# Kernel tuning notes

Measured on AMD Instinct MI355X. Metric: run time of the kernel, lower is better.

The kernel has to match this reference:

```python
import jax, jax.numpy as jnp
import numpy as np
from jax import lax

B, D, N, M = 512, 1024, 8192, 2048  # batch, input_dim, n_sdr, n_minicolumns
K = 4            # n_columns
W_SPARSE = 320   # SDR sparsity w (active bits per SDR)
K_ACTIVE = 40    # active minicolumns per step
PERM_THRESH = 0.5
LR = 0.01
CONSENSUS_THRESH = 1.0  # strict AND


def setup_inputs() -> dict:
    key = jax.random.key(0)
    k1, k2, k3 = jax.random.split(key, 3)
    s_batch = jax.random.normal(k1, (B, D), dtype=jnp.float32)
    W_enc = jax.random.normal(k2, (K, D, N), dtype=jnp.float32)  # per-column encoders (no weight sharing)
    perm = jax.random.uniform(k3, (K, M, N), dtype=jnp.float32)  # per-column permanences
    return {"s_batch": s_batch, "W_enc": W_enc, "perm": perm}


def _one_hot_topk(scores, k):
    # scores: [B, C] -> binary [B, C] with top-k per row set to 1
    _, idx = lax.top_k(scores, k)
    rows = jnp.arange(scores.shape[0])[:, None]
    return jnp.zeros_like(scores).at[rows, idx].set(1.0)


def reference(s_batch, W_enc, perm):
    def column(We, P):
        # SDRSpace.encode: random projection + top-w binarization
        scores = s_batch @ We                       # [B, N]
        sdr = _one_hot_topk(scores, W_SPARSE)       # [B, N] binary
        # SpatialPooler.forward_batch: overlap with connected synapses, top-k minicolumns
        connected = (P >= PERM_THRESH).astype(sdr.dtype)  # [M, N]
        overlap = sdr @ connected.T                 # [B, M]
        act = _one_hot_topk(overlap, K_ACTIVE)      # [B, M] binary winners
        # hebbian_update_batch: reinforce active inputs, punish inactive, on winning columns
        delta = (LR / B) * (act.T @ (2.0 * sdr - 1.0))    # [M, N] scatter-accumulated
        P_new = jnp.clip(P + delta, 0.0, 1.0)
        return sdr, P_new

    all_sdrs, perms_new = jax.vmap(column)(W_enc, perm)   # [K,B,N], [K,M,N]
    vote_fraction = all_sdrs.mean(axis=0)                  # [B, N]
    consensus = (vote_fraction >= CONSENSUS_THRESH).astype(jnp.float32)
    return consensus, all_sdrs[0], perms_new
```

## Files before the change

### kernel.cpp

```cpp
#include <hip/hip_runtime.h>
#include <stdint.h>

#define B_   512
#define D_   1024
#define N_   8192
#define M_   2048
#define K_   4
#define WSP  320
#define KACT 40
#define NW   128

typedef _Float16 f16;
typedef _Float16 f16x4 __attribute__((ext_vector_type(4)));
typedef _Float16 f16x8 __attribute__((ext_vector_type(8)));
typedef float f32x4 __attribute__((ext_vector_type(4)));

#define BM 128
#define BN 128
#define SPLIT_SCALE 2048.0f
#define SPLIT_INV (1.0f / 2048.0f)

#define GLD16(g, l) __builtin_amdgcn_global_load_lds( \
    (const __attribute__((address_space(1))) uint32_t*)(g), \
    (__attribute__((address_space(3))) uint32_t*)(l), 16, 0, 0)

__global__ __launch_bounds__(256) void conn_bits_kernel(const float* __restrict__ perm,
                                                        uint32_t* __restrict__ conn32,
                                                        int* __restrict__ mcount) {
    int km = blockIdx.x;
    int tid = threadIdx.x;
    if (tid == 0) mcount[km] = 0;
    const float* p = perm + (size_t)km * N_ + tid * 32;
    uint32_t bits = 0;
#pragma unroll
    for (int q = 0; q < 8; q++) {
        float4 v = *(const float4*)&p[q * 4];
        bits |= (v.x >= 0.5f ? 1u : 0u) << (q * 4 + 0);
        bits |= (v.y >= 0.5f ? 1u : 0u) << (q * 4 + 1);
        bits |= (v.z >= 0.5f ? 1u : 0u) << (q * 4 + 2);
        bits |= (v.w >= 0.5f ? 1u : 0u) << (q * 4 + 3);
    }
    conn32[(size_t)km * 256 + tid] = bits;
}

__global__ __launch_bounds__(256) void splitS_kernel(const float* __restrict__ S,
                                                     uint8_t* __restrict__ imgA) {
    int blk = blockIdx.x;
    int mt = blk >> 5, dstep = blk & 31;
    int tid = threadIdx.x;
    uint8_t* outb = imgA + (size_t)blk * 16384;
#pragma unroll
    for (int q = 0; q < 4; q++) {
        int o = tid * 16 + q * 4096;
        int r = o >> 7, inner = o & 127;
        int sw = (r & 7) << 4;
        int raw = inner ^ sw;
        int plane = raw >> 6;
        int k0 = (raw & 63) >> 1;
        const float* sp = &S[(size_t)(mt * 128 + r) * D_ + dstep * 32 + k0];
        float4 v0 = *(const float4*)sp;
        float4 v1 = *(const float4*)(sp + 4);
        f16x8 out;
        if (plane == 0) {
            out[0] = (f16)v0.x; out[1] = (f16)v0.y; out[2] = (f16)v0.z; out[3] = (f16)v0.w;
            out[4] = (f16)v1.x; out[5] = (f16)v1.y; out[6] = (f16)v1.z; out[7] = (f16)v1.w;
        } else {
            f16 h0 = (f16)v0.x, h1 = (f16)v0.y, h2 = (f16)v0.z, h3 = (f16)v0.w;
            f16 h4 = (f16)v1.x, h5 = (f16)v1.y, h6 = (f16)v1.z, h7 = (f16)v1.w;
            out[0] = (f16)((v0.x - (float)h0) * SPLIT_SCALE);
            out[1] = (f16)((v0.y - (float)h1) * SPLIT_SCALE);
            out[2] = (f16)((v0.z - (float)h2) * SPLIT_SCALE);
            out[3] = (f16)((v0.w - (float)h3) * SPLIT_SCALE);
            out[4] = (f16)((v1.x - (float)h4) * SPLIT_SCALE);
            out[5] = (f16)((v1.y - (float)h5) * SPLIT_SCALE);
            out[6] = (f16)((v1.z - (float)h6) * SPLIT_SCALE);
            out[7] = (f16)((v1.w - (float)h7) * SPLIT_SCALE);
        }
        *(f16x8*)&outb[o] = out;
    }
}

__device__ __forceinline__ uint32_t packHL(float x) {
    f16 h = (f16)x;
    f16 l = (f16)((x - (float)h) * SPLIT_SCALE);
    union { f16 v[2]; uint32_t u; } c;
    c.v[0] = h; c.v[1] = l;
    return c.u;
}

__global__ __launch_bounds__(256, 2) void gemm_kernel(const uint8_t* __restrict__ imgA,
                                                      const float* __restrict__ W,
                                                      float* __restrict__ C) {
    __shared__ __align__(16) uint8_t Alds[16384];
    __shared__ __align__(16) uint8_t Blds[16384];

    int bid = blockIdx.x;
    int l = (bid & 7) * 128 + (bid >> 3);
    int mt = l & 3, nt = (l >> 2) & 63, kt = l >> 8;

    int tid = threadIdx.x;
    int wave = tid >> 6, lane = tid & 63;
    int wm = wave >> 1, wn = wave & 1;
    int lr = lane & 15, lg = lane >> 4;

    const uint8_t* srcA = imgA + (size_t)(mt * 32) * 16384 + wave * 1024 + lane * 16;
    uint8_t* dstA = Alds + wave * 1024;

    const float* Wp = W + (size_t)kt * D_ * N_ + nt * BN;
    float* Cp = C + (size_t)kt * B_ * N_ + (size_t)(mt * BM) * N_ + nt * BN;

    int bn = tid & 127;
    int kc0 = tid >> 7;
    int bsw = (bn & 7) << 4;

    f32x4 acc0[4][4], acc1[4][4];
#pragma unroll
    for (int i = 0; i < 4; i++)
#pragma unroll
        for (int j = 0; j < 4; j++) {
            acc0[i][j] = (f32x4){0.f, 0.f, 0.f, 0.f};
            acc1[i][j] = (f32x4){0.f, 0.f, 0.f, 0.f};
        }

    for (int dstep = 0; dstep < 32; dstep++) {
#pragma unroll
        for (int q = 0; q < 4; q++)
            GLD16(srcA + q * 4096, dstA + q * 4096);
        srcA += 16384;
#pragma unroll
        for (int kci = 0; kci < 2; kci++) {
            int kc = kc0 + kci * 2;
            const float* wp = Wp + (size_t)(dstep * 32 + kc * 8) * N_ + bn;
            float w0 = wp[0 * N_], w1 = wp[1 * N_], w2 = wp[2 * N_], w3 = wp[3 * N_];
            float w4 = wp[4 * N_], w5 = wp[5 * N_], w6 = wp[6 * N_], w7 = wp[7 * N_];
            f16x8 hv, lv;
            hv[0] = (f16)w0; hv[1] = (f16)w1; hv[2] = (f16)w2; hv[3] = (f16)w3;
            hv[4] = (f16)w4; hv[5] = (f16)w5; hv[6] = (f16)w6; hv[7] = (f16)w7;
            lv[0] = (f16)((w0 - (float)hv[0]) * SPLIT_SCALE);
            lv[1] = (f16)((w1 - (float)hv[1]) * SPLIT_SCALE);
            lv[2] = (f16)((w2 - (float)hv[2]) * SPLIT_SCALE);
            lv[3] = (f16)((w3 - (float)hv[3]) * SPLIT_SCALE);
            lv[4] = (f16)((w4 - (float)hv[4]) * SPLIT_SCALE);
            lv[5] = (f16)((w5 - (float)hv[5]) * SPLIT_SCALE);
            lv[6] = (f16)((w6 - (float)hv[6]) * SPLIT_SCALE);
            lv[7] = (f16)((w7 - (float)hv[7]) * SPLIT_SCALE);
            *(f16x8*)&Blds[bn * 128 + ((kc * 16) ^ bsw)] = hv;
            *(f16x8*)&Blds[bn * 128 + ((64 + kc * 16) ^ bsw)] = lv;
        }
        __syncthreads();

        f16x8 ah[4], al[4];
#pragma unroll
        for (int i = 0; i < 4; i++) {
            int r = wm * 64 + i * 16 + lr;
            int sw = (r & 7) << 4;
            ah[i] = *(const f16x8*)&Alds[r * 128 + ((lg * 16) ^ sw)];
            al[i] = *(const f16x8*)&Alds[r * 128 + ((64 + lg * 16) ^ sw)];
        }
#pragma unroll
        for (int jj = 0; jj < 4; jj++) {
            int n = wn * 64 + jj * 16 + lr;
            int sw = (n & 7) << 4;
            f16x8 bh = *(const f16x8*)&Blds[n * 128 + ((lg * 16) ^ sw)];
            f16x8 bl = *(const f16x8*)&Blds[n * 128 + ((64 + lg * 16) ^ sw)];
#pragma unroll
            for (int i = 0; i < 4; i++) {
                acc0[i][jj] = __builtin_amdgcn_mfma_f32_16x16x32_f16(ah[i], bh, acc0[i][jj], 0, 0, 0);
                acc1[i][jj] = __builtin_amdgcn_mfma_f32_16x16x32_f16(ah[i], bl, acc1[i][jj], 0, 0, 0);
                acc1[i][jj] = __builtin_amdgcn_mfma_f32_16x16x32_f16(al[i], bh, acc1[i][jj], 0, 0, 0);
            }
        }
        __syncthreads();
    }
#pragma unroll
    for (int i = 0; i < 4; i++)
#pragma unroll
        for (int jj = 0; jj < 4; jj++) {
            int r0 = wm * 64 + i * 16 + lg * 4;
            int c0 = wn * 64 + jj * 16 + lr;
#pragma unroll
            for (int r = 0; r < 4; r++)
                Cp[(size_t)(r0 + r) * N_ + c0] = acc0[i][jj][r] + acc1[i][jj][r] * SPLIT_INV;
        }
}

__global__ __launch_bounds__(256) void sdr_select_kernel(const float* __restrict__ scores,
                                                         uint32_t* __restrict__ sdr_bits32) {
    __shared__ int hist[256];
    __shared__ int scan2[256];
    __shared__ uint32_t sh_prefix;
    __shared__ int sh_r;

    int b = blockIdx.x;
    int k = blockIdx.y;
    int tid = threadIdx.x;
    const float* row = scores + ((size_t)k * B_ + b) * N_ + tid * 32;

    uint32_t key[32];
#pragma unroll
    for (int q = 0; q < 8; q++) {
        float4 v = *(const float4*)&row[q * 4];
        uint32_t u0 = __float_as_uint(v.x), u1 = __float_as_uint(v.y);
        uint32_t u2 = __float_as_uint(v.z), u3 = __float_as_uint(v.w);
        key[q * 4 + 0] = (u0 & 0x80000000u) ? ~u0 : (u0 | 0x80000000u);
        key[q * 4 + 1] = (u1 & 0x80000000u) ? ~u1 : (u1 | 0x80000000u);
        key[q * 4 + 2] = (u2 & 0x80000000u) ? ~u2 : (u2 | 0x80000000u);
        key[q * 4 + 3] = (u3 & 0x80000000u) ? ~u3 : (u3 | 0x80000000u);
    }
    if (tid == 0) { sh_prefix = 0u; sh_r = WSP; }
    __syncthreads();

    for (int p = 3; p >= 0; p--) {
        hist[tid] = 0;
        __syncthreads();
        uint32_t prefix = sh_prefix;
        int r = sh_r;
        uint32_t maskHi = (p == 3) ? 0u : (0xFFFFFFFFu << ((p + 1) * 8));
        int shift = p * 8;
#pragma unroll
        for (int j = 0; j < 32; j++) {
            uint32_t u = key[j];
            if ((u & maskHi) == prefix) atomicAdd(&hist[(u >> shift) & 255], 1);
        }
        __syncthreads();
#pragma unroll
        for (int off = 1; off < 256; off <<= 1) {
            int x = hist[tid] + ((tid + off < 256) ? hist[tid + off] : 0);
            __syncthreads();
            hist[tid] = x;
            __syncthreads();
        }
        int Sv = hist[tid];
        int Sn = (tid < 255) ? hist[tid + 1] : 0;
        if (Sv >= r && Sn < r) { sh_prefix = prefix | ((uint32_t)tid << shift); sh_r = r - Sn; }
        __syncthreads();
    }
    uint32_t t = sh_prefix;

    int gt = 0, eq = 0;
#pragma unroll
    for (int j = 0; j < 32; j++) {
        gt += (key[j] > t); eq += (key[j] == t);
    }
    hist[tid] = gt; scan2[tid] = eq;
    __syncthreads();
#pragma unroll
    for (int off = 1; off < 256; off <<= 1) {
        int g = hist[tid] + ((tid >= off) ? hist[tid - off] : 0);
        int e = scan2[tid] + ((tid >= off) ? scan2[tid - off] : 0);
        __syncthreads();
        hist[tid] = g; scan2[tid] = e;
        __syncthreads();
    }
    int totalGt = hist[255];
    int eb = scan2[tid] - eq;
    int r_eq = WSP - totalGt;

    uint32_t bits = 0;
#pragma unroll
    for (int j = 0; j < 32; j++) {
        uint32_t u = key[j];
        bool f = (u > t) || ((u == t) && (eb < r_eq));
        if (u == t) eb++;
        if (f) bits |= (1u << j);
    }
    sdr_bits32[((size_t)k * B_ + b) * 256 + tid] = bits;
}

#define OV_BBLK 16
#define OV_MTILE 512
__global__ __launch_bounds__(256) void overlap_mat_kernel(const uint64_t* __restrict__ sdr_bits,
                                                          const uint64_t* __restrict__ conn,
                                                          uint16_t* __restrict__ ovmat) {
    __shared__ uint64_t sw[OV_BBLK][NW];

    int bid = blockIdx.x;
    int nb = (bid & 7) * 64 + (bid >> 3);
    int k = nb >> 7;
    int rem = nb & 127;
    int b0 = (rem >> 2) * OV_BBLK;
    int m0 = (rem & 3) * OV_MTILE;
    int tid = threadIdx.x;

    for (int i = tid; i < OV_BBLK * NW; i += 256) {
        int bb = i >> 7, w = i & 127;
        sw[bb][w] = sdr_bits[((size_t)k * B_ + b0 + bb) * NW + w];
    }
    __syncthreads();

    int m_a = m0 + tid;
    int m_b = m0 + tid + 256;
    const ulonglong2* cra = (const ulonglong2*)(conn + ((size_t)k * M_ + m_a) * NW);
    const ulonglong2* crb = (const ulonglong2*)(conn + ((size_t)k * M_ + m_b) * NW);

    int acca[OV_BBLK], accb[OV_BBLK];
#pragma unroll
    for (int i = 0; i < OV_BBLK; i++) { acca[i] = 0; accb[i] = 0; }

#pragma unroll 2
    for (int wp = 0; wp < NW / 2; wp++) {
        ulonglong2 ca = cra[wp];
        ulonglong2 cb = crb[wp];
#pragma unroll
        for (int bb = 0; bb < OV_BBLK; bb++) {
            ulonglong2 s = *(const ulonglong2*)&sw[bb][wp * 2];
            acca[bb] += __popcll(ca.x & s.x) + __popcll(ca.y & s.y);
            accb[bb] += __popcll(cb.x & s.x) + __popcll(cb.y & s.y);
        }
    }
#pragma unroll
    for (int bb = 0; bb < OV_BBLK; bb++) {
        ovmat[((size_t)k * B_ + b0 + bb) * M_ + m_a] = (uint16_t)acca[bb];
        ovmat[((size_t)k * B_ + b0 + bb) * M_ + m_b] = (uint16_t)accb[bb];
    }
}

__global__ __launch_bounds__(256) void top40_kernel(const uint16_t* __restrict__ ovmat,
                                                    int* __restrict__ mcount,
                                                    int* __restrict__ mlist) {
    __shared__ int hist[512];
    __shared__ int scanbuf[256];
    __shared__ int sh_t, sh_req;

    int kb = blockIdx.x;
    int k = kb >> 9;
    int b = kb & 511;
    int tid = threadIdx.x;

    union { uint4 raw; uint16_t v[8]; } ov;
    ov.raw = *(const uint4*)&ovmat[(size_t)kb * M_ + tid * 8];

    hist[tid] = 0; hist[tid + 256] = 0;
    __syncthreads();
#pragma unroll
    for (int j = 0; j < 8; j++) atomicAdd(&hist[ov.v[j]], 1);
    __syncthreads();
#pragma unroll
    for (int off = 1; off < 512; off <<= 1) {
        int a0 = hist[tid] + ((tid + off < 512) ? hist[tid + off] : 0);
        int a1 = hist[tid + 256] + ((tid + 256 + off < 512) ? hist[tid + 256 + off] : 0);
        __syncthreads();
        hist[tid] = a0; hist[tid + 256] = a1;
        __syncthreads();
    }
#pragma unroll
    for (int which = 0; which < 2; which++) {
        int v = tid + which * 256;
        int Sv = hist[v];
        int Sn = (v < 511) ? hist[v + 1] : 0;
        if (Sv >= KACT && Sn < KACT) { sh_t = v; sh_req = KACT - Sn; }
    }
    __syncthreads();
    int t = sh_t, req = sh_req;
    int eq = 0;
#pragma unroll
    for (int j = 0; j < 8; j++) eq += (ov.v[j] == t);
    scanbuf[tid] = eq;
    __syncthreads();
#pragma unroll
    for (int off = 1; off < 256; off <<= 1) {
        int e = scanbuf[tid] + ((tid >= off) ? scanbuf[tid - off] : 0);
        __syncthreads();
        scanbuf[tid] = e;
        __syncthreads();
    }
    int eb = scanbuf[tid] - eq;
#pragma unroll
    for (int j = 0; j < 8; j++) {
        int m = tid * 8 + j;
        int v2 = ov.v[j];
        bool act = (v2 > t) || (v2 == t && eb < req);
        if (v2 == t) eb++;
        if (act) {
            int pos = atomicAdd(&mcount[k * M_ + m], 1);
            mlist[(((size_t)k * M_ + m) << 9) + pos] = b;
        }
    }
}

__global__ void consensus_kernel(const uint64_t* __restrict__ sdr_bits,
                                 float* __restrict__ cons,
                                 float* __restrict__ sdr0) {
    int gid = blockIdx.x * 256 + threadIdx.x;
    int b = gid >> 13;
    int n = gid & (N_ - 1);
    int wi = n >> 6, bit = n & 63;
    size_t base = (size_t)b * NW + wi;
    uint64_t w0 = sdr_bits[base];
    uint64_t w1 = sdr_bits[(size_t)1 * B_ * NW + base];
    uint64_t w2 = sdr_bits[(size_t)2 * B_ * NW + base];
    uint64_t w3 = sdr_bits[(size_t)3 * B_ * NW + base];
    uint64_t a = w0 & w1 & w2 & w3;
    cons[gid] = (float)((a >> bit) & 1);
    sdr0[gid] = (float)((w0 >> bit) & 1);
}

__global__ __launch_bounds__(512) void update_kernel(const float* __restrict__ perm,
                                                     const uint64_t* __restrict__ sdr_bits,
                                                     const int* __restrict__ mcount,
                                                     const int* __restrict__ mlist,
                                                     float* __restrict__ pout) {
    __shared__ int blist[512];
    int km = blockIdx.x;
    int k = km / M_;
    int tid = threadIdx.x;
    int cnt = mcount[km];
    for (int i = tid; i < cnt; i += 512) blist[i] = mlist[((size_t)km << 9) + i];
    __syncthreads();

    int n0 = tid * 16;
    int c[16];
#pragma unroll
    for (int j = 0; j < 16; j++) c[j] = 0;
    int wi = n0 >> 6;
    int sh = n0 & 63;
    const uint64_t* sb = sdr_bits + (size_t)k * B_ * NW;
    for (int i = 0; i < cnt; i++) {
        uint64_t wv = sb[(size_t)blist[i] * NW + wi];
        unsigned bits = (unsigned)((wv >> sh) & 0xFFFFu);
#pragma unroll
        for (int j = 0; j < 16; j++) c[j] += (bits >> j) & 1;
    }
    const float scale = (float)(0.01 / 512.0);
    const float* pr = perm + (size_t)km * N_ + n0;
    float* po = pout + (size_t)km * N_ + n0;
#pragma unroll
    for (int q = 0; q < 4; q++) {
        float4 pv = *(const float4*)&pr[q * 4];
        float4 o;
        o.x = fminf(fmaxf(pv.x + scale * (float)(2 * c[q * 4 + 0] - cnt), 0.f), 1.f);
        o.y = fminf(fmaxf(pv.y + scale * (float)(2 * c[q * 4 + 1] - cnt), 0.f), 1.f);
        o.z = fminf(fmaxf(pv.z + scale * (float)(2 * c[q * 4 + 2] - cnt), 0.f), 1.f);
        o.w = fminf(fmaxf(pv.w + scale * (float)(2 * c[q * 4 + 3] - cnt), 0.f), 1.f);
        *(float4*)&po[q * 4] = o;
    }
}

extern "C" void kernel_launch(void* const* d_in, const int* in_sizes, int n_in,
                              void* d_out, int out_size, void* d_ws, size_t ws_size,
                              hipStream_t stream) {
    const float* s_batch = (const float*)d_in[0];
    const float* W_enc   = (const float*)d_in[1];
    const float* perm    = (const float*)d_in[2];

    float* out  = (float*)d_out;
    float* cons = out;
    float* sdr0 = out + (size_t)B_ * N_;
    float* pout = out + (size_t)2 * B_ * N_;

    char* ws = (char*)d_ws;
    float*    scores   = (float*)ws;
    uint16_t* ovmat    = (uint16_t*)ws;
    uint64_t* sdr_bits = (uint64_t*)(ws + ((size_t)64 << 20));
    uint64_t* conn     = (uint64_t*)(ws + ((size_t)66 << 20));
    int*      mcount   = (int*)(ws + ((size_t)74 << 20));
    int*      mlist    = (int*)(ws + ((size_t)75 << 20));
    uint8_t*  imgA     = (uint8_t*)(ws + ((size_t)92 << 20));

    conn_bits_kernel<<<K_ * M_, 256, 0, stream>>>(perm, (uint32_t*)conn, mcount);

    splitS_kernel<<<4 * 32, 256, 0, stream>>>(s_batch, imgA);

    gemm_kernel<<<K_ * (B_ / BM) * (N_ / BN), 256, 0, stream>>>(imgA, W_enc, scores);

    dim3 gs(B_, K_);
    sdr_select_kernel<<<gs, 256, 0, stream>>>(scores, (uint32_t*)sdr_bits);

    overlap_mat_kernel<<<K_ * (B_ / OV_BBLK) * (M_ / OV_MTILE), 256, 0, stream>>>(
        sdr_bits, conn, ovmat);
    top40_kernel<<<K_ * B_, 256, 0, stream>>>(ovmat, mcount, mlist);

    consensus_kernel<<<(B_ * N_) / 256, 256, 0, stream>>>(sdr_bits, cons, sdr0);
    update_kernel<<<K_ * M_, 512, 0, stream>>>(perm, sdr_bits, mcount, mlist, pout);
}
```

Before: 474.0 us.

## Double-buffer the split-f16 GEMM with wider tiles and merge small launches

```diff
diff --git a/kernel.cpp b/kernel.cpp
--- a/kernel.cpp
+++ b/kernel.cpp
@@ -16,7 +16,7 @@
 typedef float f32x4 __attribute__((ext_vector_type(4)));
 
 #define BM 128
-#define BN 128
+#define BN 256
 #define SPLIT_SCALE 2048.0f
 #define SPLIT_INV (1.0f / 2048.0f)
 
@@ -24,11 +24,49 @@
     (const __attribute__((address_space(1))) uint32_t*)(g), \
     (__attribute__((address_space(3))) uint32_t*)(l), 16, 0, 0)
 
-__global__ __launch_bounds__(256) void conn_bits_kernel(const float* __restrict__ perm,
-                                                        uint32_t* __restrict__ conn32,
-                                                        int* __restrict__ mcount) {
-    int km = blockIdx.x;
-    int tid = threadIdx.x;
+__global__ __launch_bounds__(256) void prep_kernel(const float* __restrict__ perm,
+                                                   uint32_t* __restrict__ conn32,
+                                                   int* __restrict__ mcount,
+                                                   const float* __restrict__ S,
+                                                   uint8_t* __restrict__ imgA) {
+    int bid = blockIdx.x;
+    int tid = threadIdx.x;
+    if (bid < 128) {
+        int blk = bid;
+        int mt = blk >> 5, dstep = blk & 31;
+        uint8_t* outb = imgA + (size_t)blk * 16384;
+#pragma unroll
+        for (int q = 0; q < 4; q++) {
+            int o = tid * 16 + q * 4096;
+            int r = o >> 7, inner = o & 127;
+            int sw = (r & 7) << 4;
+            int raw = inner ^ sw;
+            int plane = raw >> 6;
+            int k0 = (raw & 63) >> 1;
+            const float* sp = &S[(size_t)(mt * 128 + r) * D_ + dstep * 32 + k0];
+            float4 v0 = *(const float4*)sp;
+            float4 v1 = *(const float4*)(sp + 4);
+            f16x8 out;
+            if (plane == 0) {
+                out[0] = (f16)v0.x; out[1] = (f16)v0.y; out[2] = (f16)v0.z; out[3] = (f16)v0.w;
+                out[4] = (f16)v1.x; out[5] = (f16)v1.y; out[6] = (f16)v1.z; out[7] = (f16)v1.w;
+            } else {
+                f16 h0 = (f16)v0.x, h1 = (f16)v0.y, h2 = (f16)v0.z, h3 = (f16)v0.w;
+                f16 h4 = (f16)v1.x, h5 = (f16)v1.y, h6 = (f16)v1.z, h7 = (f16)v1.w;
+                out[0] = (f16)((v0.x - (float)h0) * SPLIT_SCALE);
+                out[1] = (f16)((v0.y - (float)h1) * SPLIT_SCALE);
+                out[2] = (f16)((v0.z - (float)h2) * SPLIT_SCALE);
+                out[3] = (f16)((v0.w - (float)h3) * SPLIT_SCALE);
+                out[4] = (f16)((v1.x - (float)h4) * SPLIT_SCALE);
+                out[5] = (f16)((v1.y - (float)h5) * SPLIT_SCALE);
+                out[6] = (f16)((v1.z - (float)h6) * SPLIT_SCALE);
+                out[7] = (f16)((v1.w - (float)h7) * SPLIT_SCALE);
+            }
+            *(f16x8*)&outb[o] = out;
+        }
+        return;
+    }
+    int km = bid - 128;
     if (tid == 0) mcount[km] = 0;
     const float* p = perm + (size_t)km * N_ + tid * 32;
     uint32_t bits = 0;
@@ -43,74 +81,45 @@
     conn32[(size_t)km * 256 + tid] = bits;
 }
 
-__global__ __launch_bounds__(256) void splitS_kernel(const float* __restrict__ S,
-                                                     uint8_t* __restrict__ imgA) {
-    int blk = blockIdx.x;
-    int mt = blk >> 5, dstep = blk & 31;
-    int tid = threadIdx.x;
-    uint8_t* outb = imgA + (size_t)blk * 16384;
-#pragma unroll
-    for (int q = 0; q < 4; q++) {
-        int o = tid * 16 + q * 4096;
-        int r = o >> 7, inner = o & 127;
-        int sw = (r & 7) << 4;
-        int raw = inner ^ sw;
-        int plane = raw >> 6;
-        int k0 = (raw & 63) >> 1;
-        const float* sp = &S[(size_t)(mt * 128 + r) * D_ + dstep * 32 + k0];
-        float4 v0 = *(const float4*)sp;
-        float4 v1 = *(const float4*)(sp + 4);
-        f16x8 out;
-        if (plane == 0) {
-            out[0] = (f16)v0.x; out[1] = (f16)v0.y; out[2] = (f16)v0.z; out[3] = (f16)v0.w;
-            out[4] = (f16)v1.x; out[5] = (f16)v1.y; out[6] = (f16)v1.z; out[7] = (f16)v1.w;
-        } else {
-            f16 h0 = (f16)v0.x, h1 = (f16)v0.y, h2 = (f16)v0.z, h3 = (f16)v0.w;
-            f16 h4 = (f16)v1.x, h5 = (f16)v1.y, h6 = (f16)v1.z, h7 = (f16)v1.w;
-            out[0] = (f16)((v0.x - (float)h0) * SPLIT_SCALE);
-            out[1] = (f16)((v0.y - (float)h1) * SPLIT_SCALE);
-            out[2] = (f16)((v0.z - (float)h2) * SPLIT_SCALE);
-            out[3] = (f16)((v0.w - (float)h3) * SPLIT_SCALE);
-            out[4] = (f16)((v1.x - (float)h4) * SPLIT_SCALE);
-            out[5] = (f16)((v1.y - (float)h5) * SPLIT_SCALE);
-            out[6] = (f16)((v1.z - (float)h6) * SPLIT_SCALE);
-            out[7] = (f16)((v1.w - (float)h7) * SPLIT_SCALE);
-        }
-        *(f16x8*)&outb[o] = out;
-    }
-}
-
-__device__ __forceinline__ uint32_t packHL(float x) {
-    f16 h = (f16)x;
-    f16 l = (f16)((x - (float)h) * SPLIT_SCALE);
-    union { f16 v[2]; uint32_t u; } c;
-    c.v[0] = h; c.v[1] = l;
-    return c.u;
-}
-
-__global__ __launch_bounds__(256, 2) void gemm_kernel(const uint8_t* __restrict__ imgA,
+__device__ __forceinline__ void pack_write_B(uint8_t* Bn, const float* w,
+                                             int kc0, int bn, int bsw) {
+#pragma unroll
+    for (int kci = 0; kci < 2; kci++) {
+        int kc = kc0 * 2 + kci;
+        f16x8 hv, lv;
+#pragma unroll
+        for (int j = 0; j < 8; j++) {
+            float x = w[kci * 8 + j];
+            f16 h = (f16)x;
+            hv[j] = h;
+            lv[j] = (f16)((x - (float)h) * SPLIT_SCALE);
+        }
+        *(f16x8*)&Bn[bn * 128 + ((kc * 16) ^ bsw)] = hv;
+        *(f16x8*)&Bn[bn * 128 + ((64 + kc * 16) ^ bsw)] = lv;
+    }
+}
+
+__global__ __launch_bounds__(512, 2) void gemm_kernel(const uint8_t* __restrict__ imgA,
                                                       const float* __restrict__ W,
                                                       float* __restrict__ C) {
-    __shared__ __align__(16) uint8_t Alds[16384];
-    __shared__ __align__(16) uint8_t Blds[16384];
+    __shared__ __align__(16) uint8_t lds[98304];
 
     int bid = blockIdx.x;
-    int l = (bid & 7) * 128 + (bid >> 3);
-    int mt = l & 3, nt = (l >> 2) & 63, kt = l >> 8;
+    int l = (bid & 7) * 64 + (bid >> 3);
+    int mt = l & 3, nt = (l >> 2) & 31, kt = l >> 7;
 
     int tid = threadIdx.x;
     int wave = tid >> 6, lane = tid & 63;
-    int wm = wave >> 1, wn = wave & 1;
+    int wm = wave >> 2, wn = wave & 3;
     int lr = lane & 15, lg = lane >> 4;
 
-    const uint8_t* srcA = imgA + (size_t)(mt * 32) * 16384 + wave * 1024 + lane * 16;
-    uint8_t* dstA = Alds + wave * 1024;
+    const uint8_t* srcA0 = imgA + (size_t)(mt * 32) * 16384 + wave * 1024 + lane * 16;
 
     const float* Wp = W + (size_t)kt * D_ * N_ + nt * BN;
     float* Cp = C + (size_t)kt * B_ * N_ + (size_t)(mt * BM) * N_ + nt * BN;
 
-    int bn = tid & 127;
-    int kc0 = tid >> 7;
+    int bn = tid & 255;
+    int kc0 = tid >> 8;
     int bsw = (bn & 7) << 4;
 
     f32x4 acc0[4][4], acc1[4][4];
@@ -122,56 +131,65 @@
             acc1[i][j] = (f32x4){0.f, 0.f, 0.f, 0.f};
         }
 
+    {
+        uint8_t* dA = lds + wave * 1024;
+        GLD16(srcA0, dA);
+        GLD16(srcA0 + 8192, dA + 8192);
+        float w[16];
+        const float* wp0 = Wp + (size_t)(kc0 * 16) * N_ + bn;
+#pragma unroll
+        for (int j = 0; j < 16; j++) w[j] = wp0[(size_t)j * N_];
+        pack_write_B(lds + 32768, w, kc0, bn, bsw);
+    }
+    __syncthreads();
+
     for (int dstep = 0; dstep < 32; dstep++) {
-#pragma unroll
-        for (int q = 0; q < 4; q++)
-            GLD16(srcA + q * 4096, dstA + q * 4096);
-        srcA += 16384;
-#pragma unroll
-        for (int kci = 0; kci < 2; kci++) {
-            int kc = kc0 + kci * 2;
-            const float* wp = Wp + (size_t)(dstep * 32 + kc * 8) * N_ + bn;
-            float w0 = wp[0 * N_], w1 = wp[1 * N_], w2 = wp[2 * N_], w3 = wp[3 * N_];
-            float w4 = wp[4 * N_], w5 = wp[5 * N_], w6 = wp[6 * N_], w7 = wp[7 * N_];
-            f16x8 hv, lv;
-            hv[0] = (f16)w0; hv[1] = (f16)w1; hv[2] = (f16)w2; hv[3] = (f16)w3;
-            hv[4] = (f16)w4; hv[5] = (f16)w5; hv[6] = (f16)w6; hv[7] = (f16)w7;
-            lv[0] = (f16)((w0 - (float)hv[0]) * SPLIT_SCALE);
-            lv[1] = (f16)((w1 - (float)hv[1]) * SPLIT_SCALE);
-            lv[2] = (f16)((w2 - (float)hv[2]) * SPLIT_SCALE);
-            lv[3] = (f16)((w3 - (float)hv[3]) * SPLIT_SCALE);
-            lv[4] = (f16)((w4 - (float)hv[4]) * SPLIT_SCALE);
-            lv[5] = (f16)((w5 - (float)hv[5]) * SPLIT_SCALE);
-            lv[6] = (f16)((w6 - (float)hv[6]) * SPLIT_SCALE);
-            lv[7] = (f16)((w7 - (float)hv[7]) * SPLIT_SCALE);
-            *(f16x8*)&Blds[bn * 128 + ((kc * 16) ^ bsw)] = hv;
-            *(f16x8*)&Blds[bn * 128 + ((64 + kc * 16) ^ bsw)] = lv;
-        }
-        __syncthreads();
+        int cur = dstep & 1;
+        uint8_t* Ac = lds + cur * 16384;
+        uint8_t* Bc = lds + 32768 + cur * 32768;
+        bool pf = (dstep < 31);
+
+        float wreg[16];
+        if (pf) {
+            const uint8_t* sA = srcA0 + (size_t)(dstep + 1) * 16384;
+            uint8_t* dA = lds + (cur ^ 1) * 16384 + wave * 1024;
+            GLD16(sA, dA);
+            GLD16(sA + 8192, dA + 8192);
+            const float* wp0 = Wp + (size_t)((dstep + 1) * 32 + kc0 * 16) * N_ + bn;
+#pragma unroll
+            for (int j = 0; j < 16; j++) wreg[j] = wp0[(size_t)j * N_];
+        }
 
         f16x8 ah[4], al[4];
 #pragma unroll
         for (int i = 0; i < 4; i++) {
             int r = wm * 64 + i * 16 + lr;
             int sw = (r & 7) << 4;
-            ah[i] = *(const f16x8*)&Alds[r * 128 + ((lg * 16) ^ sw)];
-            al[i] = *(const f16x8*)&Alds[r * 128 + ((64 + lg * 16) ^ sw)];
+            ah[i] = *(const f16x8*)&Ac[r * 128 + ((lg * 16) ^ sw)];
+            al[i] = *(const f16x8*)&Ac[r * 128 + ((64 + lg * 16) ^ sw)];
         }
 #pragma unroll
         for (int jj = 0; jj < 4; jj++) {
             int n = wn * 64 + jj * 16 + lr;
             int sw = (n & 7) << 4;
-            f16x8 bh = *(const f16x8*)&Blds[n * 128 + ((lg * 16) ^ sw)];
-            f16x8 bl = *(const f16x8*)&Blds[n * 128 + ((64 + lg * 16) ^ sw)];
+            f16x8 bh = *(const f16x8*)&Bc[n * 128 + ((lg * 16) ^ sw)];
+            f16x8 bl = *(const f16x8*)&Bc[n * 128 + ((64 + lg * 16) ^ sw)];
+            __builtin_amdgcn_s_setprio(1);
 #pragma unroll
             for (int i = 0; i < 4; i++) {
                 acc0[i][jj] = __builtin_amdgcn_mfma_f32_16x16x32_f16(ah[i], bh, acc0[i][jj], 0, 0, 0);
                 acc1[i][jj] = __builtin_amdgcn_mfma_f32_16x16x32_f16(ah[i], bl, acc1[i][jj], 0, 0, 0);
                 acc1[i][jj] = __builtin_amdgcn_mfma_f32_16x16x32_f16(al[i], bh, acc1[i][jj], 0, 0, 0);
             }
-        }
-        __syncthreads();
-    }
+            __builtin_amdgcn_s_setprio(0);
+        }
+
+        if (pf)
+            pack_write_B(lds + 32768 + (cur ^ 1) * 32768, wreg, kc0, bn, bsw);
+
+        __syncthreads();
+    }
+
 #pragma unroll
     for (int i = 0; i < 4; i++)
 #pragma unroll
@@ -378,29 +396,29 @@
     }
 }
 
-__global__ void consensus_kernel(const uint64_t* __restrict__ sdr_bits,
-                                 float* __restrict__ cons,
-                                 float* __restrict__ sdr0) {
-    int gid = blockIdx.x * 256 + threadIdx.x;
-    int b = gid >> 13;
-    int n = gid & (N_ - 1);
-    int wi = n >> 6, bit = n & 63;
-    size_t base = (size_t)b * NW + wi;
-    uint64_t w0 = sdr_bits[base];
-    uint64_t w1 = sdr_bits[(size_t)1 * B_ * NW + base];
-    uint64_t w2 = sdr_bits[(size_t)2 * B_ * NW + base];
-    uint64_t w3 = sdr_bits[(size_t)3 * B_ * NW + base];
-    uint64_t a = w0 & w1 & w2 & w3;
-    cons[gid] = (float)((a >> bit) & 1);
-    sdr0[gid] = (float)((w0 >> bit) & 1);
-}
-
-__global__ __launch_bounds__(512) void update_kernel(const float* __restrict__ perm,
-                                                     const uint64_t* __restrict__ sdr_bits,
-                                                     const int* __restrict__ mcount,
-                                                     const int* __restrict__ mlist,
-                                                     float* __restrict__ pout) {
+__global__ __launch_bounds__(512) void tail_kernel(const float* __restrict__ perm,
+                                                   const uint64_t* __restrict__ sdr_bits,
+                                                   const int* __restrict__ mcount,
+                                                   const int* __restrict__ mlist,
+                                                   float* __restrict__ pout,
+                                                   float* __restrict__ cons,
+                                                   float* __restrict__ sdr0) {
     __shared__ int blist[512];
+    if (blockIdx.x >= 8192) {
+        int gid = (blockIdx.x - 8192) * 512 + threadIdx.x;
+        int b = gid >> 13;
+        int n = gid & (N_ - 1);
+        int wi = n >> 6, bit = n & 63;
+        size_t base = (size_t)b * NW + wi;
+        uint64_t w0 = sdr_bits[base];
+        uint64_t w1 = sdr_bits[(size_t)1 * B_ * NW + base];
+        uint64_t w2 = sdr_bits[(size_t)2 * B_ * NW + base];
+        uint64_t w3 = sdr_bits[(size_t)3 * B_ * NW + base];
+        uint64_t a = w0 & w1 & w2 & w3;
+        cons[gid] = (float)((a >> bit) & 1);
+        sdr0[gid] = (float)((w0 >> bit) & 1);
+        return;
+    }
     int km = blockIdx.x;
     int k = km / M_;
     int tid = threadIdx.x;
@@ -457,11 +475,10 @@
     int*      mlist    = (int*)(ws + ((size_t)75 << 20));
     uint8_t*  imgA     = (uint8_t*)(ws + ((size_t)92 << 20));
 
-    conn_bits_kernel<<<K_ * M_, 256, 0, stream>>>(perm, (uint32_t*)conn, mcount);
-
-    splitS_kernel<<<4 * 32, 256, 0, stream>>>(s_batch, imgA);
-
-    gemm_kernel<<<K_ * (B_ / BM) * (N_ / BN), 256, 0, stream>>>(imgA, W_enc, scores);
+    prep_kernel<<<8192 + 128, 256, 0, stream>>>(perm, (uint32_t*)conn, mcount,
+                                                s_batch, imgA);
+
+    gemm_kernel<<<K_ * (B_ / BM) * (N_ / BN), 512, 0, stream>>>(imgA, W_enc, scores);
 
     dim3 gs(B_, K_);
     sdr_select_kernel<<<gs, 256, 0, stream>>>(scores, (uint32_t*)sdr_bits);
@@ -470,6 +487,6 @@
         sdr_bits, conn, ovmat);
     top40_kernel<<<K_ * B_, 256, 0, stream>>>(ovmat, mcount, mlist);
 
-    consensus_kernel<<<(B_ * N_) / 256, 256, 0, stream>>>(sdr_bits, cons, sdr0);
-    update_kernel<<<K_ * M_, 512, 0, stream>>>(perm, sdr_bits, mcount, mlist, pout);
-}
+    tail_kernel<<<16384, 512, 0, stream>>>(perm, sdr_bits, mcount, mlist,
+                                           pout, cons, sdr0);
+}
```

Measured after the change: 450.5 us. 5.0% less time.
